# Optimization experiments

Hardware: AMD Instinct MI355X
Metric: run time of the kernel (lower is better)

## Reference

```python
import jax, jax.numpy as jnp
import numpy as np

B, S, D_MODEL = 8, 1024, 512
DIM_K = DIM_V = 512
N_HEADS = 8
DK = DIM_K // N_HEADS
DV = DIM_V // N_HEADS
NORM = 1.0 / np.sqrt(D_MODEL).astype(np.float32)  # note: 1/sqrt(d_model), per source


def setup_inputs() -> dict:
    key = jax.random.key(0)
    ks = jax.random.split(key, 6)
    s = 0.05  # small init to keep softmax well-conditioned
    return {
        "x": jax.random.normal(ks[0], (B, S, D_MODEL), jnp.float32),
        "y": jax.random.normal(ks[1], (B, S, D_MODEL), jnp.float32),
        "q_w": jax.random.normal(ks[2], (D_MODEL, DIM_K), jnp.float32) * s,
        "q_b": jnp.zeros((DIM_K,), jnp.float32),
        "k_w": jax.random.normal(ks[3], (D_MODEL, DIM_K), jnp.float32) * s,
        "k_b": jnp.zeros((DIM_K,), jnp.float32),
        "v_w": jax.random.normal(ks[4], (D_MODEL, DIM_V), jnp.float32) * s,
        "v_b": jnp.zeros((DIM_V,), jnp.float32),
        "o_w": jax.random.normal(ks[5], (DIM_V, D_MODEL), jnp.float32) * s,
        "o_b": jnp.zeros((D_MODEL,), jnp.float32),
    }


def reference(x, y, q_w, q_b, k_w, k_b, v_w, v_b, o_w, o_b):
    b, s, _ = x.shape
    # Faithful to torch: plain row-major reshape (B,S,dim) -> (H,B,S,dh),
    # NOT a per-token head split.
    Q = (x @ q_w + q_b).reshape(N_HEADS, b, s, DK)
    K = (y @ k_w + k_b).reshape(N_HEADS, b, s, DK)
    V = (y @ v_w + v_b).reshape(N_HEADS, b, s, DV)
    scores = jnp.einsum("hbqd,hbkd->hbqk", Q, K) * NORM  # [H,B,S,S]
    # dynamic mean-threshold mask: keep only scores strictly above row mean
    thre = jnp.mean(scores, axis=-1, keepdims=True)
    scores = jnp.where(scores > thre, scores, -jnp.inf)
    attn = jax.nn.softmax(scores, axis=-1)
    out = jnp.einsum("hbqk,hbkd->hbqd", attn, V).reshape(b, s, DIM_V)
    return out @ o_w + o_b
```

## Files before the change

kernel.cpp:

```cpp
#include <hip/hip_runtime.h>
#include <hip/hip_bf16.h>
#include <hip/hip_fp16.h>


typedef _Float16 f16;
typedef __attribute__((ext_vector_type(4))) _Float16 f16x4;
typedef __attribute__((ext_vector_type(8))) _Float16 f16x8;
typedef __attribute__((ext_vector_type(8))) short bf16x8;
typedef __attribute__((ext_vector_type(4))) float f32x4;

#define MFMA16(a, b, c) __builtin_amdgcn_mfma_f32_16x16x32_f16((a), (b), (c), 0, 0, 0)
#define MFMAB16(a, b, c) __builtin_amdgcn_mfma_f32_16x16x32_bf16((a), (b), (c), 0, 0, 0)
#define MFMAPV(a, b, c) __builtin_amdgcn_mfma_f32_16x16x16f16((a), (b), (c), 0, 0, 0)

#if defined(__has_builtin) && __has_builtin(__builtin_amdgcn_exp2f)
#define EXPFN(x) __builtin_amdgcn_exp2f(x)
#define QPROJ_SCALE (0.04419417382415922f * 1.4426950408889634f)
#else
#define EXPFN(x) __expf(x)
#define QPROJ_SCALE 0.04419417382415922f
#endif

#define GLL16(gp, lp)                                       \
  __builtin_amdgcn_global_load_lds(                         \
      (const __attribute__((address_space(1))) void*)(gp),  \
      (__attribute__((address_space(3))) void*)(lp), 16, 0, 0)

__device__ __forceinline__ float b2f(short s) {
  return __uint_as_float(((unsigned)(unsigned short)s) << 16);
}

__device__ __forceinline__ void splitbf(float v, short& h, short& l) {
  unsigned short hu = __bfloat16_as_ushort(__float2bfloat16(v));
  h = (short)hu;
  float hf = __uint_as_float(((unsigned)hu) << 16);
  l = (short)__bfloat16_as_ushort(__float2bfloat16(v - hf));
}

__global__ void k_wt(const float* __restrict__ w0, const float* __restrict__ w1,
                     const float* __restrict__ w2, const float* __restrict__ w3,
                     short* __restrict__ qh, short* __restrict__ ql,
                     short* __restrict__ kh, short* __restrict__ kl,
                     f16* __restrict__ vt, f16* __restrict__ ot) {
  const float* W;
  switch (blockIdx.z) {
    case 0: W = w0; break;
    case 1: W = w1; break;
    case 2: W = w2; break;
    default: W = w3; break;
  }
  __shared__ float t[32][33];
  int bx = blockIdx.x, by = blockIdx.y;
  int tx = threadIdx.x, ty = threadIdx.y;
#pragma unroll
  for (int i = 0; i < 32; i += 8)
    t[ty + i][tx] = W[(size_t)(by * 32 + ty + i) * 512 + bx * 32 + tx];
  __syncthreads();
#pragma unroll
  for (int i = 0; i < 32; i += 8) {
    size_t idx = (size_t)(bx * 32 + ty + i) * 512 + by * 32 + tx;
    float v = t[tx][ty + i];
    if (blockIdx.z < 2) {
      short h, l;
      splitbf(v, h, l);
      if (blockIdx.z == 0) { qh[idx] = h; ql[idx] = l; }
      else { kh[idx] = h; kl[idx] = l; }
    } else {
      if (blockIdx.z == 2) vt[idx] = (f16)v;
      else ot[idx] = (f16)v;
    }
  }
}

__global__ __launch_bounds__(256) void k_split(
    const float* __restrict__ x, const float* __restrict__ y,
    short* __restrict__ Xh, short* __restrict__ Xl, short* __restrict__ Yh,
    short* __restrict__ Yl, f16* __restrict__ Ym) {
  const float* src = blockIdx.y ? y : x;
  short* dh = blockIdx.y ? Yh : Xh;
  short* dl = blockIdx.y ? Yl : Xl;
  const size_t i = ((size_t)blockIdx.x * 256 + threadIdx.x) * 8;
  float4 a = *(const float4*)(src + i);
  float4 b = *(const float4*)(src + i + 4);
  float v[8] = {a.x, a.y, a.z, a.w, b.x, b.y, b.z, b.w};
  bf16x8 h, l;
#pragma unroll
  for (int j = 0; j < 8; ++j) {
    short hh, ll;
    splitbf(v[j], hh, ll);
    h[j] = hh;
    l[j] = ll;
  }
  *(bf16x8*)(dh + i) = h;
  *(bf16x8*)(dl + i) = l;
  if (blockIdx.y) {
    f16x8 m8;
#pragma unroll
    for (int j = 0; j < 8; ++j) m8[j] = (f16)v[j];
    *(f16x8*)(Ym + i) = m8;
  }
}

#define GSTAGE(buf, kk)                                              \
  {                                                                  \
    _Pragma("unroll") for (int j = 0; j < 4; ++j) {                  \
      const int rowu = half + j * 16;                                \
      const int row = rowu + srow;                                   \
      const int slog = sslot ^ ((row >> 1) & 3);                     \
      GLL16(gsb + (size_t)(rb + row) * 512 + (kk) + slog * 8,        \
            &ldsb[buf][rowu][0]);                                    \
    }                                                                \
  }

template <typename OT>
__device__ __forceinline__ void gemm16_gll(const f16* __restrict__ A,
                                           const f16* __restrict__ WT,
                                           const float* __restrict__ bias,
                                           OT* __restrict__ C, int m0, int n0,
                                           f16 (*As)[128][32],
                                           f16 (*Bs)[128][32]) {
  const int tid = threadIdx.x;
  const int wv = tid >> 6, lane = tid & 63;
  const int wm = wv >> 1, wn = wv & 1;
  const int l15 = lane & 15, lg = lane >> 4;
  const int srow = lane >> 2, sslot = lane & 3;

  const f16* gsb = (wv < 2) ? A : WT;
  const int rb = (wv < 2) ? m0 : n0;
  f16(*ldsb)[128][32] = (wv < 2) ? As : Bs;
  const int half = (wv & 1) * 64;

  const f32x4 fz = {0.f, 0.f, 0.f, 0.f};
  f32x4 acc[4][4];
#pragma unroll
  for (int m = 0; m < 4; ++m)
#pragma unroll
    for (int n = 0; n < 4; ++n) acc[m][n] = fz;

  GSTAGE(0, 0);
  int cur = 0;
  for (int k0 = 0; k0 < 512; k0 += 32) {
    __syncthreads();
    if (k0 < 480) GSTAGE(cur ^ 1, k0 + 32);
    f16x8 af[4], bf[4];
#pragma unroll
    for (int m = 0; m < 4; ++m) {
      const int r = wm * 64 + m * 16 + l15;
      af[m] = *(const f16x8*)&As[cur][r][(lg ^ ((r >> 1) & 3)) * 8];
    }
#pragma unroll
    for (int n = 0; n < 4; ++n) {
      const int r = wn * 64 + n * 16 + l15;
      bf[n] = *(const f16x8*)&Bs[cur][r][(lg ^ ((r >> 1) & 3)) * 8];
    }
#pragma unroll
    for (int m = 0; m < 4; ++m)
#pragma unroll
      for (int n = 0; n < 4; ++n) acc[m][n] = MFMA16(af[m], bf[n], acc[m][n]);
    cur ^= 1;
  }
#pragma unroll
  for (int n = 0; n < 4; ++n) {
    const int col = n0 + wn * 64 + n * 16 + l15;
    const float b = bias[col];
#pragma unroll
    for (int m = 0; m < 4; ++m) {
      const int row = m0 + wm * 64 + m * 16 + lg * 4;
#pragma unroll
      for (int r = 0; r < 4; ++r)
        C[(size_t)(row + r) * 512 + col] = (OT)(acc[m][n][r] + b);
    }
  }
}

__global__ __launch_bounds__(256) void k_gemm_out(const f16* __restrict__ Om,
                                                  const f16* __restrict__ owT,
                                                  const float* __restrict__ ob,
                                                  float* __restrict__ out) {
  __shared__ __align__(16) f16 As[2][128][32];
  __shared__ __align__(16) f16 Bs[2][128][32];
  const int lid = blockIdx.x + (blockIdx.y << 2);
  const int swz = ((lid & 7) << 5) + (lid >> 3);
  gemm16_gll<float>(Om, owT, ob, out, (swz >> 2) * 128, (swz & 3) * 128, As,
                    Bs);
}

#define PSTAGE(buf, kk)                                             \
  {                                                                 \
    _Pragma("unroll") for (int j = 0; j < 8; ++j) {                 \
      const int row = j * 16 + srow;                                \
      const int slog = sslot ^ ((row >> 1) & 3);                    \
      GLL16(gsb + (size_t)(rb + row) * 512 + (kk) + slog * 8,       \
            &sm4[buf][wv][j * 16][0]);                              \
    }                                                               \
  }

__global__ __launch_bounds__(256) void k_proj(
    const short* __restrict__ Xh, const short* __restrict__ Xl,
    const short* __restrict__ Yh, const short* __restrict__ Yl,
    const f16* __restrict__ Ym, const short* __restrict__ qwh,
    const short* __restrict__ qwl, const short* __restrict__ kwh,
    const short* __restrict__ kwl, const f16* __restrict__ vwT,
    const float* __restrict__ qb, const float* __restrict__ kbias,
    const float* __restrict__ vb, short* __restrict__ Qh,
    short* __restrict__ Ql, short* __restrict__ Kh, short* __restrict__ Kl,
    f16* __restrict__ Vm, float* __restrict__ Kpart) {
  __shared__ __align__(16) short sm4[2][4][128][32];
  const int lid = blockIdx.x + (blockIdx.y << 2);
  const int swz = ((lid & 7) << 5) + (lid >> 3);
  const int nt = swz & 3, mt = swz >> 2;
  const int m0 = mt * 128, n0 = nt * 128;
  const int z = blockIdx.z;
  if (z == 2) {
    gemm16_gll<f16>(Ym, vwT, vb, Vm, m0, n0, (f16(*)[128][32]) & sm4[0][0][0][0],
                    (f16(*)[128][32]) & sm4[0][2][0][0]);
    return;
  }
  const short* Agh = z ? Yh : Xh;
  const short* Agl = z ? Yl : Xl;
  const short* Wh = z ? kwh : qwh;
  const short* Wl = z ? kwl : qwl;
  const float* bias = z ? kbias : qb;
  short* Ch = z ? Kh : Qh;
  short* Cl = z ? Kl : Ql;
  const float osc = z ? 1.f : (float)QPROJ_SCALE;

  const int tid = threadIdx.x;
  const int wv = tid >> 6, lane = tid & 63;
  const int wm = wv >> 1, wn = wv & 1;
  const int l15 = lane & 15, lg = lane >> 4;
  const int srow = lane >> 2, sslot = lane & 3;

  const short* gsb = (wv == 0) ? Agh : (wv == 1) ? Agl : (wv == 2) ? Wh : Wl;
  const int rb = (wv < 2) ? m0 : n0;

  const f32x4 fz = {0.f, 0.f, 0.f, 0.f};
  f32x4 acc[4][4];
#pragma unroll
  for (int m = 0; m < 4; ++m)
#pragma unroll
    for (int n = 0; n < 4; ++n) acc[m][n] = fz;

  PSTAGE(0, 0);
  int cur = 0;
  for (int k0 = 0; k0 < 512; k0 += 32) {
    __syncthreads();
    if (k0 < 480) PSTAGE(cur ^ 1, k0 + 32);
    bf16x8 afh[4], afl[4], bfh[4], bfl[4];
#pragma unroll
    for (int m = 0; m < 4; ++m) {
      const int r = wm * 64 + m * 16 + l15;
      const int sl = (lg ^ ((r >> 1) & 3)) * 8;
      afh[m] = *(const bf16x8*)&sm4[cur][0][r][sl];
      afl[m] = *(const bf16x8*)&sm4[cur][1][r][sl];
    }
#pragma unroll
    for (int n = 0; n < 4; ++n) {
      const int r = wn * 64 + n * 16 + l15;
      const int sl = (lg ^ ((r >> 1) & 3)) * 8;
      bfh[n] = *(const bf16x8*)&sm4[cur][2][r][sl];
      bfl[n] = *(const bf16x8*)&sm4[cur][3][r][sl];
    }
#pragma unroll
    for (int m = 0; m < 4; ++m)
#pragma unroll
      for (int n = 0; n < 4; ++n) {
        acc[m][n] = MFMAB16(afh[m], bfh[n], acc[m][n]);
        acc[m][n] = MFMAB16(afh[m], bfl[n], acc[m][n]);
        acc[m][n] = MFMAB16(afl[m], bfh[n], acc[m][n]);
      }
    cur ^= 1;
  }
  float csum[4];
#pragma unroll
  for (int n = 0; n < 4; ++n) {
    const int col = n0 + wn * 64 + n * 16 + l15;
    const float b = bias[col];
    csum[n] = 16.f * b;
#pragma unroll
    for (int m = 0; m < 4; ++m) {
      const int row = m0 + wm * 64 + m * 16 + lg * 4;
#pragma unroll
      for (int r = 0; r < 4; ++r) {
        const float vraw = acc[m][n][r] + b;
        csum[n] += acc[m][n][r];
        short h, l;
        splitbf(vraw * osc, h, l);
        const size_t idx = (size_t)(row + r) * 512 + col;
        Ch[idx] = h;
        Cl[idx] = l;
      }
    }
  }
  if (z == 1) {
    float* cred = (float*)&sm4[0][0][0][0];
    __syncthreads();
#pragma unroll
    for (int n = 0; n < 4; ++n)
      cred[(wn * 64 + n * 16 + l15) * 8 + wm * 4 + lg] = csum[n];
    __syncthreads();
    if (tid < 64) {
      float s = 0.f;
#pragma unroll
      for (int j = 0; j < 8; ++j)
        s += cred[tid * 8 + j] + cred[(tid + 64) * 8 + j];
      Kpart[((size_t)mt * 4 + nt) * 64 + tid] = s;
    }
  }
}

__global__ __launch_bounds__(256) void k_vtr(const f16* __restrict__ Vm,
                                             f16* __restrict__ Vt) {
  const int p = blockIdx.y;
  const int j0 = blockIdx.x * 16;
  __shared__ f16 L[16][520];
  const int tid = threadIdx.x;
#pragma unroll
  for (int it = 0; it < 4; ++it) {
    int idx = it * 256 + tid;
    int row = idx >> 6, oct = idx & 63;
    *(f16x8*)&L[row][oct * 8] =
        *(const f16x8*)&Vm[(size_t)(p * 128 + j0 + row) * 512 + oct * 8];
  }
  __syncthreads();
#pragma unroll
  for (int it = 0; it < 4; ++it) {
    int idx = it * 256 + tid;
    int dh = idx >> 4, j = idx & 15;
    f16x8 v;
#pragma unroll
    for (int g = 0; g < 8; ++g) v[g] = L[j][g * 64 + dh];
    *(f16x8*)&Vt[((size_t)p * 64 + dh) * 1024 + (j0 + j) * 8] = v;
  }
}

#define LOADREG(cc)                              \
  {                                              \
    rh = *(const bf16x8*)(KhSrc + (cc) * 4096);  \
    rl = *(const bf16x8*)(KlSrc + (cc) * 4096);  \
    rv = *(const f16x8*)(VSrc + (cc) * 64);      \
  }
#define STOREBUF(b)                      \
  {                                      \
    *(bf16x8*)&KhS[b][skey][sslot] = rh; \
    *(bf16x8*)&KlS[b][skey][sslot] = rl; \
    *(f16x8*)&Vs[b][skey][sslot] = rv;   \
  }

__global__ __launch_bounds__(512, 4) void k_attn(
    const short* __restrict__ Qh, const short* __restrict__ Ql,
    const short* __restrict__ Kh, const short* __restrict__ Kl,
    const f16* __restrict__ Vt, const float* __restrict__ Kpart,
    f16* __restrict__ Om) {
  constexpr int S = 1024, DH = 64;
  const int p = blockIdx.x;
  const int qt = blockIdx.y;
  const size_t pb = (size_t)p * S * DH;
  const short* Qhp = Qh + pb;
  const short* Qlp = Ql + pb;
  const short* Khp = Kh + pb;
  const short* Klp = Kl + pb;
  const f16* Vtp = Vt + pb;
  f16* Op = Om + pb;

  const int tid = threadIdx.x;
  const int w = tid >> 6, lane = tid & 63;
  const int l15 = lane & 15, lg = lane >> 4;

  __shared__ __align__(16) short KhS[2][64][64];
  __shared__ __align__(16) short KlS[2][64][64];
  __shared__ __align__(16) f16 Vs[2][64][64];

  const int skey = tid >> 3;
  const int slot8 = tid & 7;
  const int sslot = (slot8 ^ (skey & 7)) * 8;
  const short* KhSrc = Khp + skey * 64 + slot8 * 8;
  const short* KlSrc = Klp + skey * 64 + slot8 * 8;
  const f16* VSrc = Vtp + (size_t)skey * 1024 + slot8 * 8;

  bf16x8 rh, rl;
  f16x8 rv;
  LOADREG(0);
  STOREBUF(0);
  LOADREG(1);

  const int qrow = qt * 128 + w * 16;
  const size_t qo = (size_t)(qrow + l15) * DH + lg * 8;
  bf16x8 qh0 = *(const bf16x8*)(Qhp + qo);
  bf16x8 ql0 = *(const bf16x8*)(Qlp + qo);
  bf16x8 qh1 = *(const bf16x8*)(Qhp + qo + 32);
  bf16x8 ql1 = *(const bf16x8*)(Qlp + qo + 32);

  const float* kp = Kpart + (size_t)p * 256;
  float km0[8], km1[8];
#pragma unroll
  for (int j = 0; j < 8; ++j) { km0[j] = 0.f; km1[j] = 0.f; }
#pragma unroll
  for (int pt = 0; pt < 4; ++pt) {
    const float* bb = kp + pt * 64;
#pragma unroll
    for (int j = 0; j < 8; ++j) {
      km0[j] += bb[lg * 8 + j];
      km1[j] += bb[32 + lg * 8 + j];
    }
  }
  float sm = 0.f;
#pragma unroll
  for (int j = 0; j < 8; ++j) {
    sm += (b2f(qh0[j]) + b2f(ql0[j])) * km0[j] +
          (b2f(qh1[j]) + b2f(ql1[j])) * km1[j];
  }
  sm += __shfl_xor(sm, 16);
  sm += __shfl_xor(sm, 32);
  sm *= (1.f / 1024.f);

  const f32x4 fz = {0.f, 0.f, 0.f, 0.f};
  const f16x4 kones = {(f16)1.f, (f16)1.f, (f16)1.f, (f16)1.f};
  f32x4 oac[4];
#pragma unroll
  for (int d = 0; d < 4; ++d) oac[d] = fz;
  f32x4 od = fz;

  for (int c = 0; c < 16; ++c) {
    __syncthreads();
    const int cb = c & 1;
    if (c < 15) STOREBUF(cb ^ 1);
    if (c < 14) LOADREG(c + 2);
    __builtin_amdgcn_s_setprio(1);
#pragma unroll
    for (int t = 0; t < 4; ++t) {
      const int krow = t * 16 + l15;
      const int ksw = krow & 7;
      bf16x8 kh0 = *(const bf16x8*)&KhS[cb][krow][(lg ^ ksw) * 8];
      bf16x8 kh1 = *(const bf16x8*)&KhS[cb][krow][((4 + lg) ^ ksw) * 8];
      bf16x8 kl0 = *(const bf16x8*)&KlS[cb][krow][(lg ^ ksw) * 8];
      bf16x8 kl1 = *(const bf16x8*)&KlS[cb][krow][((4 + lg) ^ ksw) * 8];
      f32x4 a = fz;
      a = MFMAB16(kh0, qh0, a);
      a = MFMAB16(kh1, qh1, a);
      a = MFMAB16(kh0, ql0, a);
      a = MFMAB16(kl0, qh0, a);
      a = MFMAB16(kh1, ql1, a);
      a = MFMAB16(kl1, qh1, a);
      f16x4 pf;
#pragma unroll
      for (int r = 0; r < 4; ++r) {
        float v = a[r];
        float e = (v > sm) ? EXPFN(v) : 0.f;
        pf[r] = (f16)e;
      }
      od = MFMAPV(kones, pf, od);
#pragma unroll
      for (int d0 = 0; d0 < 4; ++d0) {
        const int vrow = d0 * 16 + l15;
        const int vsw = vrow & 7;
        f16x4 va = *(const f16x4*)&Vs[cb][vrow]
                                     [(((t * 2 + (lg >> 1)) ^ vsw) * 8) +
                                      (lg & 1) * 4];
        oac[d0] = MFMAPV(va, pf, oac[d0]);
      }
    }
    __builtin_amdgcn_s_setprio(0);
  }

  const float inv = 1.f / od[0];
#pragma unroll
  for (int d0 = 0; d0 < 4; ++d0) {
    f16x4 o0;
#pragma unroll
    for (int r = 0; r < 4; ++r) o0[r] = (f16)(oac[d0][r] * inv);
    *(f16x4*)&Op[(size_t)(qrow + l15) * DH + d0 * 16 + lg * 4] = o0;
  }
}

extern "C" void kernel_launch(void* const* d_in, const int* in_sizes, int n_in,
                              void* d_out, int out_size, void* d_ws,
                              size_t ws_size, hipStream_t stream) {
  const float* x = (const float*)d_in[0];
  const float* y = (const float*)d_in[1];
  const float* qw = (const float*)d_in[2];
  const float* qb = (const float*)d_in[3];
  const float* kw = (const float*)d_in[4];
  const float* kbias = (const float*)d_in[5];
  const float* vw = (const float*)d_in[6];
  const float* vb = (const float*)d_in[7];
  const float* ow = (const float*)d_in[8];
  const float* ob = (const float*)d_in[9];
  float* out = (float*)d_out;

  char* ws = (char*)d_ws;
  const size_t WT_B = 512ull * 512 * 2;
  const size_t MAT_B = 8192ull * 512 * 2;
  short* qwhT = (short*)(ws + 0 * WT_B);
  short* qwlT = (short*)(ws + 1 * WT_B);
  short* kwhT = (short*)(ws + 2 * WT_B);
  short* kwlT = (short*)(ws + 3 * WT_B);
  f16* vwT = (f16*)(ws + 4 * WT_B);
  f16* owT = (f16*)(ws + 5 * WT_B);
  char* m = ws + 6 * WT_B;
  short* Qh = (short*)(m + 0 * MAT_B);
  short* Ql = (short*)(m + 1 * MAT_B);
  short* Kh = (short*)(m + 2 * MAT_B);
  short* Kl = (short*)(m + 3 * MAT_B);
  f16* Vm = (f16*)(m + 4 * MAT_B);
  short* Xh = (short*)(m + 5 * MAT_B);
  short* Xl = (short*)(m + 6 * MAT_B);
  short* Yh = (short*)(m + 7 * MAT_B);
  short* Yl = (short*)(m + 8 * MAT_B);
  f16* Ym = (f16*)(m + 9 * MAT_B);
  float* Kpart = (float*)(m + 10 * MAT_B);
  f16* Vtr = (f16*)Xh;
  f16* Om = (f16*)Yh;

  hipLaunchKernelGGL(k_wt, dim3(16, 16, 4), dim3(32, 8), 0, stream, qw, kw, vw,
                     ow, qwhT, qwlT, kwhT, kwlT, vwT, owT);
  hipLaunchKernelGGL(k_split, dim3(2048, 2), dim3(256), 0, stream, x, y, Xh,
                     Xl, Yh, Yl, Ym);
  hipLaunchKernelGGL(k_proj, dim3(4, 64, 3), dim3(256), 0, stream, Xh, Xl, Yh,
                     Yl, Ym, qwhT, qwlT, kwhT, kwlT, vwT, qb, kbias, vb, Qh,
                     Ql, Kh, Kl, Vm, Kpart);
  hipLaunchKernelGGL(k_vtr, dim3(8, 64), dim3(256), 0, stream, Vm, Vtr);
  hipLaunchKernelGGL(k_attn, dim3(64, 8), dim3(512), 0, stream, Qh, Ql, Kh, Kl,
                     Vtr, Kpart, Om);
  hipLaunchKernelGGL(k_gemm_out, dim3(4, 64), dim3(256), 0, stream, Om, owT,
                     ob, out);
}
```

Baseline: 118.9 us.

## Process two query tiles per wave in attention to reuse K/V LDS fragments

The attention kernel now runs 256 threads per block, with each wave handling 32 query rows (two 16-row tiles) instead of 16. Each K and V fragment read from LDS feeds two sets of MFMAs, which halves LDS read traffic per unit of work. Each thread now stages twice as much K/V data per chunk. The chunk loop is manually unrolled by two so the double-buffer index is a compile-time constant. The cost is higher register pressure and fewer waves per block, which may reduce latency hiding.

```diff
diff --git a/kernel.cpp b/kernel.cpp
--- a/kernel.cpp
+++ b/kernel.cpp
@@ -334,20 +334,76 @@
   }
 }
 
-#define LOADREG(cc)                              \
-  {                                              \
-    rh = *(const bf16x8*)(KhSrc + (cc) * 4096);  \
-    rl = *(const bf16x8*)(KlSrc + (cc) * 4096);  \
-    rv = *(const f16x8*)(VSrc + (cc) * 64);      \
-  }
-#define STOREBUF(b)                      \
-  {                                      \
-    *(bf16x8*)&KhS[b][skey][sslot] = rh; \
-    *(bf16x8*)&KlS[b][skey][sslot] = rl; \
-    *(f16x8*)&Vs[b][skey][sslot] = rv;   \
-  }
-
-__global__ __launch_bounds__(512, 4) void k_attn(
+#define LOADREG(cc)                                   \
+  {                                                   \
+    rh0 = *(const bf16x8*)(KhSrc + (cc) * 4096);      \
+    rh1 = *(const bf16x8*)(KhSrc + (cc) * 4096 + 8);  \
+    rl0 = *(const bf16x8*)(KlSrc + (cc) * 4096);      \
+    rl1 = *(const bf16x8*)(KlSrc + (cc) * 4096 + 8);  \
+    rv0 = *(const f16x8*)(VSrc + (cc) * 64);          \
+    rv1 = *(const f16x8*)(VSrc + (cc) * 64 + 8);      \
+  }
+#define STOREBUF(b)                        \
+  {                                        \
+    *(bf16x8*)&KhS[b][skey][sslot0] = rh0; \
+    *(bf16x8*)&KhS[b][skey][sslot1] = rh1; \
+    *(bf16x8*)&KlS[b][skey][sslot0] = rl0; \
+    *(bf16x8*)&KlS[b][skey][sslot1] = rl1; \
+    *(f16x8*)&Vs[b][skey][sslot0] = rv0;   \
+    *(f16x8*)&Vs[b][skey][sslot1] = rv1;   \
+  }
+
+#define CHUNK(cb_, c_)                                                        \
+  {                                                                           \
+    __syncthreads();                                                          \
+    if ((c_) < 15) STOREBUF((cb_) ^ 1);             \
+    if ((c_) < 14) LOADREG((c_) + 2);                                         \
+    __builtin_amdgcn_s_setprio(1);                                            \
+    _Pragma("unroll") for (int t = 0; t < 4; ++t) {                           \
+      const int krow = t * 16 + l15;                                          \
+      const int ksw = l15 & 7;            \
+      bf16x8 kh0 = *(const bf16x8*)&KhS[cb_][krow][(lg ^ ksw) * 8];           \
+      bf16x8 kh1 = *(const bf16x8*)&KhS[cb_][krow][((4 + lg) ^ ksw) * 8];     \
+      bf16x8 kl0 = *(const bf16x8*)&KlS[cb_][krow][(lg ^ ksw) * 8];           \
+      bf16x8 kl1 = *(const bf16x8*)&KlS[cb_][krow][((4 + lg) ^ ksw) * 8];     \
+      f32x4 a0 = fz, a1 = fz;                                                 \
+      a0 = MFMAB16(kh0, q0h0, a0);                                            \
+      a0 = MFMAB16(kh1, q0h1, a0);                                            \
+      a0 = MFMAB16(kh0, q0l0, a0);                                            \
+      a0 = MFMAB16(kl0, q0h0, a0);                                            \
+      a0 = MFMAB16(kh1, q0l1, a0);                                            \
+      a0 = MFMAB16(kl1, q0h1, a0);                                            \
+      a1 = MFMAB16(kh0, q1h0, a1);                                            \
+      a1 = MFMAB16(kh1, q1h1, a1);                                            \
+      a1 = MFMAB16(kh0, q1l0, a1);                                            \
+      a1 = MFMAB16(kl0, q1h0, a1);                                            \
+      a1 = MFMAB16(kh1, q1l1, a1);                                            \
+      a1 = MFMAB16(kl1, q1h1, a1);                                            \
+      f16x4 pf0, pf1;                                                         \
+      _Pragma("unroll") for (int r = 0; r < 4; ++r) {                         \
+        float v0 = a0[r];                                                     \
+        float e0 = (v0 > sm0) ? EXPFN(v0) : 0.f;                              \
+        pf0[r] = (f16)e0;                                                     \
+        float v1 = a1[r];                                                     \
+        float e1 = (v1 > sm1) ? EXPFN(v1) : 0.f;                              \
+        pf1[r] = (f16)e1;                                                     \
+      }                                                                       \
+      od0 = MFMAPV(kones, pf0, od0);                                          \
+      od1 = MFMAPV(kones, pf1, od1);                                          \
+      _Pragma("unroll") for (int d0 = 0; d0 < 4; ++d0) {                      \
+        const int vrow = d0 * 16 + l15;                                       \
+        const int vsw = l15 & 7;                                              \
+        f16x4 va = *(const f16x4*)&Vs[cb_][vrow]                              \
+                                      [(((t * 2 + (lg >> 1)) ^ vsw) * 8) +    \
+                                       (lg & 1) * 4];                         \
+        oac0[d0] = MFMAPV(va, pf0, oac0[d0]);                                 \
+        oac1[d0] = MFMAPV(va, pf1, oac1[d0]);                                 \
+      }                                                                       \
+    }                                                                         \
+    __builtin_amdgcn_s_setprio(0);                                            \
+  }
+
+__global__ __launch_bounds__(256, 3) void k_attn(
     const short* __restrict__ Qh, const short* __restrict__ Ql,
     const short* __restrict__ Kh, const short* __restrict__ Kl,
     const f16* __restrict__ Vt, const float* __restrict__ Kpart,
@@ -371,25 +427,32 @@
   __shared__ __align__(16) short KlS[2][64][64];
   __shared__ __align__(16) f16 Vs[2][64][64];
 
-  const int skey = tid >> 3;
-  const int slot8 = tid & 7;
-  const int sslot = (slot8 ^ (skey & 7)) * 8;
-  const short* KhSrc = Khp + skey * 64 + slot8 * 8;
-  const short* KlSrc = Klp + skey * 64 + slot8 * 8;
-  const f16* VSrc = Vtp + (size_t)skey * 1024 + slot8 * 8;
-
-  bf16x8 rh, rl;
-  f16x8 rv;
+  const int skey = tid >> 2;
+  const int s2 = (tid & 3) * 2;
+  const int ssw = skey & 7;
+  const int sslot0 = (s2 ^ ssw) * 8;
+  const int sslot1 = ((s2 + 1) ^ ssw) * 8;
+  const short* KhSrc = Khp + skey * 64 + (tid & 3) * 16;
+  const short* KlSrc = Klp + skey * 64 + (tid & 3) * 16;
+  const f16* VSrc = Vtp + (size_t)skey * 1024 + (tid & 3) * 16;
+
+  bf16x8 rh0, rh1, rl0, rl1;
+  f16x8 rv0, rv1;
   LOADREG(0);
   STOREBUF(0);
   LOADREG(1);
 
-  const int qrow = qt * 128 + w * 16;
-  const size_t qo = (size_t)(qrow + l15) * DH + lg * 8;
-  bf16x8 qh0 = *(const bf16x8*)(Qhp + qo);
-  bf16x8 ql0 = *(const bf16x8*)(Qlp + qo);
-  bf16x8 qh1 = *(const bf16x8*)(Qhp + qo + 32);
-  bf16x8 ql1 = *(const bf16x8*)(Qlp + qo + 32);
+  const int qrow = qt * 128 + w * 32;
+  const size_t qo0 = (size_t)(qrow + l15) * DH + lg * 8;
+  const size_t qo1 = (size_t)(qrow + 16 + l15) * DH + lg * 8;
+  bf16x8 q0h0 = *(const bf16x8*)(Qhp + qo0);
+  bf16x8 q0l0 = *(const bf16x8*)(Qlp + qo0);
+  bf16x8 q0h1 = *(const bf16x8*)(Qhp + qo0 + 32);
+  bf16x8 q0l1 = *(const bf16x8*)(Qlp + qo0 + 32);
+  bf16x8 q1h0 = *(const bf16x8*)(Qhp + qo1);
+  bf16x8 q1l0 = *(const bf16x8*)(Qlp + qo1);
+  bf16x8 q1h1 = *(const bf16x8*)(Qhp + qo1 + 32);
+  bf16x8 q1l1 = *(const bf16x8*)(Qlp + qo1 + 32);
 
   const float* kp = Kpart + (size_t)p * 256;
   float km0[8], km1[8];
@@ -404,72 +467,43 @@
       km1[j] += bb[32 + lg * 8 + j];
     }
   }
-  float sm = 0.f;
+  float sm0 = 0.f, sm1 = 0.f;
 #pragma unroll
   for (int j = 0; j < 8; ++j) {
-    sm += (b2f(qh0[j]) + b2f(ql0[j])) * km0[j] +
-          (b2f(qh1[j]) + b2f(ql1[j])) * km1[j];
-  }
-  sm += __shfl_xor(sm, 16);
-  sm += __shfl_xor(sm, 32);
-  sm *= (1.f / 1024.f);
+    sm0 += (b2f(q0h0[j]) + b2f(q0l0[j])) * km0[j] +
+           (b2f(q0h1[j]) + b2f(q0l1[j])) * km1[j];
+    sm1 += (b2f(q1h0[j]) + b2f(q1l0[j])) * km0[j] +
+           (b2f(q1h1[j]) + b2f(q1l1[j])) * km1[j];
+  }
+  sm0 += __shfl_xor(sm0, 16); sm0 += __shfl_xor(sm0, 32);
+  sm1 += __shfl_xor(sm1, 16); sm1 += __shfl_xor(sm1, 32);
+  sm0 *= (1.f / 1024.f);
+  sm1 *= (1.f / 1024.f);
 
   const f32x4 fz = {0.f, 0.f, 0.f, 0.f};
   const f16x4 kones = {(f16)1.f, (f16)1.f, (f16)1.f, (f16)1.f};
-  f32x4 oac[4];
-#pragma unroll
-  for (int d = 0; d < 4; ++d) oac[d] = fz;
-  f32x4 od = fz;
-
-  for (int c = 0; c < 16; ++c) {
-    __syncthreads();
-    const int cb = c & 1;
-    if (c < 15) STOREBUF(cb ^ 1);
-    if (c < 14) LOADREG(c + 2);
-    __builtin_amdgcn_s_setprio(1);
-#pragma unroll
-    for (int t = 0; t < 4; ++t) {
-      const int krow = t * 16 + l15;
-      const int ksw = krow & 7;
-      bf16x8 kh0 = *(const bf16x8*)&KhS[cb][krow][(lg ^ ksw) * 8];
-      bf16x8 kh1 = *(const bf16x8*)&KhS[cb][krow][((4 + lg) ^ ksw) * 8];
-      bf16x8 kl0 = *(const bf16x8*)&KlS[cb][krow][(lg ^ ksw) * 8];
-      bf16x8 kl1 = *(const bf16x8*)&KlS[cb][krow][((4 + lg) ^ ksw) * 8];
-      f32x4 a = fz;
-      a = MFMAB16(kh0, qh0, a);
-      a = MFMAB16(kh1, qh1, a);
-      a = MFMAB16(kh0, ql0, a);
-      a = MFMAB16(kl0, qh0, a);
-      a = MFMAB16(kh1, ql1, a);
-      a = MFMAB16(kl1, qh1, a);
-      f16x4 pf;
-#pragma unroll
-      for (int r = 0; r < 4; ++r) {
-        float v = a[r];
-        float e = (v > sm) ? EXPFN(v) : 0.f;
-        pf[r] = (f16)e;
-      }
-      od = MFMAPV(kones, pf, od);
-#pragma unroll
-      for (int d0 = 0; d0 < 4; ++d0) {
-        const int vrow = d0 * 16 + l15;
-        const int vsw = vrow & 7;
-        f16x4 va = *(const f16x4*)&Vs[cb][vrow]
-                                     [(((t * 2 + (lg >> 1)) ^ vsw) * 8) +
-                                      (lg & 1) * 4];
-        oac[d0] = MFMAPV(va, pf, oac[d0]);
-      }
-    }
-    __builtin_amdgcn_s_setprio(0);
-  }
-
-  const float inv = 1.f / od[0];
+  f32x4 oac0[4], oac1[4];
+#pragma unroll
+  for (int d = 0; d < 4; ++d) { oac0[d] = fz; oac1[d] = fz; }
+  f32x4 od0 = fz, od1 = fz;
+
+  for (int cc = 0; cc < 16; cc += 2) {
+    CHUNK(0, cc);
+    CHUNK(1, cc + 1);
+  }
+
+  const float inv0 = 1.f / od0[0];
+  const float inv1 = 1.f / od1[0];
 #pragma unroll
   for (int d0 = 0; d0 < 4; ++d0) {
-    f16x4 o0;
-#pragma unroll
-    for (int r = 0; r < 4; ++r) o0[r] = (f16)(oac[d0][r] * inv);
+    f16x4 o0, o1;
+#pragma unroll
+    for (int r = 0; r < 4; ++r) {
+      o0[r] = (f16)(oac0[d0][r] * inv0);
+      o1[r] = (f16)(oac1[d0][r] * inv1);
+    }
     *(f16x4*)&Op[(size_t)(qrow + l15) * DH + d0 * 16 + lg * 4] = o0;
+    *(f16x4*)&Op[(size_t)(qrow + 16 + l15) * DH + d0 * 16 + lg * 4] = o1;
   }
 }
 
@@ -520,7 +554,7 @@
                      Yl, Ym, qwhT, qwlT, kwhT, kwlT, vwT, qb, kbias, vb, Qh,
                      Ql, Kh, Kl, Vm, Kpart);
   hipLaunchKernelGGL(k_vtr, dim3(8, 64), dim3(256), 0, stream, Vm, Vtr);
-  hipLaunchKernelGGL(k_attn, dim3(64, 8), dim3(512), 0, stream, Qh, Ql, Kh, Kl,
+  hipLaunchKernelGGL(k_attn, dim3(64, 8), dim3(256), 0, stream, Qh, Ql, Kh, Kl,
                      Vtr, Kpart, Om);
   hipLaunchKernelGGL(k_gemm_out, dim3(4, 64), dim3(256), 0, stream, Om, owT,
                      ob, out);
```

New measurement: 119.9 us. About the same (+0.8%).

## Halve attention block size and key chunk, unroll double-buffer loop

Applied to the files above, without the earlier changes.

The attention kernel now uses 256-thread blocks covering 64 query rows instead of 512 threads covering 128, which doubles the grid to 1024 blocks. Each pipeline step stages 32 keys instead of 64, so shared memory per block shrinks and the loop runs 32 steps. The loop is manually unrolled by two so buffer indices are compile-time constants, and the LDS swizzles are adjusted for the new tile shapes. In exchange, each K/V tile is reused by half as many query rows, so total K/V global traffic doubles, and there are twice as many barriers per block.

```diff
diff --git a/kernel.cpp b/kernel.cpp
--- a/kernel.cpp
+++ b/kernel.cpp
@@ -334,20 +334,59 @@
   }
 }
 
-#define LOADREG(cc)                              \
-  {                                              \
-    rh = *(const bf16x8*)(KhSrc + (cc) * 4096);  \
-    rl = *(const bf16x8*)(KlSrc + (cc) * 4096);  \
-    rv = *(const f16x8*)(VSrc + (cc) * 64);      \
-  }
-#define STOREBUF(b)                      \
-  {                                      \
-    *(bf16x8*)&KhS[b][skey][sslot] = rh; \
-    *(bf16x8*)&KlS[b][skey][sslot] = rl; \
-    *(f16x8*)&Vs[b][skey][sslot] = rv;   \
-  }
-
-__global__ __launch_bounds__(512, 4) void k_attn(
+#define LOADREG(cc)                                   \
+  {                                                   \
+    rh = *(const bf16x8*)(KhSrc + (cc) * 2048);       \
+    rl = *(const bf16x8*)(KlSrc + (cc) * 2048);       \
+    rv = *(const f16x8*)(VSrc + (cc) * 32);           \
+  }
+#define STOREBUF(b)                       \
+  {                                       \
+    *(bf16x8*)&KhS[b][skey][skslot] = rh; \
+    *(bf16x8*)&KlS[b][skey][skslot] = rl; \
+    *(f16x8*)&Vs[b][sdh][svslot] = rv;    \
+  }
+
+#define CHUNK(cb_, c_)                                                        \
+  {                                                                           \
+    __syncthreads();                                                          \
+    if ((c_) < 31) STOREBUF((cb_) ^ 1);             \
+    if ((c_) < 30) LOADREG((c_) + 2);                                         \
+    __builtin_amdgcn_s_setprio(1);                                            \
+    _Pragma("unroll") for (int t = 0; t < 2; ++t) {                           \
+      const int krow = t * 16 + l15;                                          \
+      const int ksw = l15 & 7;                           \
+      bf16x8 kh0 = *(const bf16x8*)&KhS[cb_][krow][(lg ^ ksw) * 8];           \
+      bf16x8 kh1 = *(const bf16x8*)&KhS[cb_][krow][((4 + lg) ^ ksw) * 8];     \
+      bf16x8 kl0 = *(const bf16x8*)&KlS[cb_][krow][(lg ^ ksw) * 8];           \
+      bf16x8 kl1 = *(const bf16x8*)&KlS[cb_][krow][((4 + lg) ^ ksw) * 8];     \
+      f32x4 a0 = fz;                                                          \
+      a0 = MFMAB16(kh0, qh0, a0);                                             \
+      a0 = MFMAB16(kh1, qh1, a0);                                             \
+      a0 = MFMAB16(kh0, ql0, a0);                                             \
+      a0 = MFMAB16(kl0, qh0, a0);                                             \
+      a0 = MFMAB16(kh1, ql1, a0);                                             \
+      a0 = MFMAB16(kl1, qh1, a0);                                             \
+      f16x4 pf;                                                               \
+      _Pragma("unroll") for (int r = 0; r < 4; ++r) {                         \
+        float v = a0[r];                                                      \
+        float e = (v > sm) ? EXPFN(v) : 0.f;                                  \
+        pf[r] = (f16)e;                                                       \
+      }                                                                       \
+      od = MFMAPV(kones, pf, od);                                             \
+      _Pragma("unroll") for (int d0 = 0; d0 < 4; ++d0) {                      \
+        const int vrow = d0 * 16 + l15;                                       \
+        const int vsw = l15 & 3;                         \
+        f16x4 va = *(const f16x4*)&Vs[cb_][vrow]                              \
+                                      [(((t * 2 + (lg >> 1)) ^ vsw) * 8) +    \
+                                       (lg & 1) * 4];                         \
+        oac[d0] = MFMAPV(va, pf, oac[d0]);                                    \
+      }                                                                       \
+    }                                                                         \
+    __builtin_amdgcn_s_setprio(0);                                            \
+  }
+
+__global__ __launch_bounds__(256, 4) void k_attn(
     const short* __restrict__ Qh, const short* __restrict__ Ql,
     const short* __restrict__ Kh, const short* __restrict__ Kl,
     const f16* __restrict__ Vt, const float* __restrict__ Kpart,
@@ -367,16 +406,19 @@
   const int w = tid >> 6, lane = tid & 63;
   const int l15 = lane & 15, lg = lane >> 4;
 
-  __shared__ __align__(16) short KhS[2][64][64];
-  __shared__ __align__(16) short KlS[2][64][64];
-  __shared__ __align__(16) f16 Vs[2][64][64];
+  __shared__ __align__(16) short KhS[2][32][64];
+  __shared__ __align__(16) short KlS[2][32][64];
+  __shared__ __align__(16) f16 Vs[2][64][32];
 
   const int skey = tid >> 3;
-  const int slot8 = tid & 7;
-  const int sslot = (slot8 ^ (skey & 7)) * 8;
-  const short* KhSrc = Khp + skey * 64 + slot8 * 8;
-  const short* KlSrc = Klp + skey * 64 + slot8 * 8;
-  const f16* VSrc = Vtp + (size_t)skey * 1024 + slot8 * 8;
+  const int sk8 = tid & 7;
+  const int skslot = (sk8 ^ (skey & 7)) * 8;
+  const int sdh = tid >> 2;
+  const int sv4 = tid & 3;
+  const int svslot = (sv4 ^ (sdh & 3)) * 8;
+  const short* KhSrc = Khp + skey * 64 + sk8 * 8;
+  const short* KlSrc = Klp + skey * 64 + sk8 * 8;
+  const f16* VSrc = Vtp + (size_t)sdh * 1024 + sv4 * 8;
 
   bf16x8 rh, rl;
   f16x8 rv;
@@ -384,7 +426,7 @@
   STOREBUF(0);
   LOADREG(1);
 
-  const int qrow = qt * 128 + w * 16;
+  const int qrow = qt * 64 + w * 16;
   const size_t qo = (size_t)(qrow + l15) * DH + lg * 8;
   bf16x8 qh0 = *(const bf16x8*)(Qhp + qo);
   bf16x8 ql0 = *(const bf16x8*)(Qlp + qo);
@@ -421,46 +463,9 @@
   for (int d = 0; d < 4; ++d) oac[d] = fz;
   f32x4 od = fz;
 
-  for (int c = 0; c < 16; ++c) {
-    __syncthreads();
-    const int cb = c & 1;
-    if (c < 15) STOREBUF(cb ^ 1);
-    if (c < 14) LOADREG(c + 2);
-    __builtin_amdgcn_s_setprio(1);
-#pragma unroll
-    for (int t = 0; t < 4; ++t) {
-      const int krow = t * 16 + l15;
-      const int ksw = krow & 7;
-      bf16x8 kh0 = *(const bf16x8*)&KhS[cb][krow][(lg ^ ksw) * 8];
-      bf16x8 kh1 = *(const bf16x8*)&KhS[cb][krow][((4 + lg) ^ ksw) * 8];
-      bf16x8 kl0 = *(const bf16x8*)&KlS[cb][krow][(lg ^ ksw) * 8];
-      bf16x8 kl1 = *(const bf16x8*)&KlS[cb][krow][((4 + lg) ^ ksw) * 8];
-      f32x4 a = fz;
-      a = MFMAB16(kh0, qh0, a);
-      a = MFMAB16(kh1, qh1, a);
-      a = MFMAB16(kh0, ql0, a);
-      a = MFMAB16(kl0, qh0, a);
-      a = MFMAB16(kh1, ql1, a);
-      a = MFMAB16(kl1, qh1, a);
-      f16x4 pf;
-#pragma unroll
-      for (int r = 0; r < 4; ++r) {
-        float v = a[r];
-        float e = (v > sm) ? EXPFN(v) : 0.f;
-        pf[r] = (f16)e;
-      }
-      od = MFMAPV(kones, pf, od);
-#pragma unroll
-      for (int d0 = 0; d0 < 4; ++d0) {
-        const int vrow = d0 * 16 + l15;
-        const int vsw = vrow & 7;
-        f16x4 va = *(const f16x4*)&Vs[cb][vrow]
-                                     [(((t * 2 + (lg >> 1)) ^ vsw) * 8) +
-                                      (lg & 1) * 4];
-        oac[d0] = MFMAPV(va, pf, oac[d0]);
-      }
-    }
-    __builtin_amdgcn_s_setprio(0);
+  for (int cc = 0; cc < 32; cc += 2) {
+    CHUNK(0, cc);
+    CHUNK(1, cc + 1);
   }
 
   const float inv = 1.f / od[0];
@@ -520,8 +525,8 @@
                      Yl, Ym, qwhT, qwlT, kwhT, kwlT, vwT, qb, kbias, vb, Qh,
                      Ql, Kh, Kl, Vm, Kpart);
   hipLaunchKernelGGL(k_vtr, dim3(8, 64), dim3(256), 0, stream, Vm, Vtr);
-  hipLaunchKernelGGL(k_attn, dim3(64, 8), dim3(512), 0, stream, Qh, Ql, Kh, Kl,
-                     Vtr, Kpart, Om);
+  hipLaunchKernelGGL(k_attn, dim3(64, 16), dim3(256), 0, stream, Qh, Ql, Kh,
+                     Kl, Vtr, Kpart, Om);
   hipLaunchKernelGGL(k_gemm_out, dim3(4, 64), dim3(256), 0, stream, Om, owT,
                      ob, out);
 }
```

Measured after the change: 132.2 us. 11.2% more time.
